# Performance work log

Hardware: AMD Instinct MI355X
Metric: run time of the kernel (lower is better)

Reference implementation:

```python
import jax, jax.numpy as jnp
import numpy as np

N_NODES = 100000
N_EDGES = 1600000
IN_DIM = 512
H0 = 32   # hiddens[0]
H1 = 8    # hiddens[1]
DH = 8    # denoise_hidden_1
ZETA = 1.01
GAMMA = 0.0


def _gcn_conv(x, row, col, edge_weight, W, b, num_nodes):
    """PyG GCNConv: add self-loops (weight 1), symmetric normalization, X@W aggregation."""
    xw = x @ W  # [N, out]
    loops = jnp.arange(num_nodes)
    r = jnp.concatenate([row, loops])
    c = jnp.concatenate([col, loops])
    w = jnp.concatenate([edge_weight, jnp.ones((num_nodes,), x.dtype)])
    deg = jax.ops.segment_sum(w, c, num_segments=num_nodes)  # degree at target nodes
    dinv = jnp.where(deg > 0, jax.lax.rsqrt(deg), 0.0)
    norm = dinv[r] * w * dinv[c]                  # [E+N]
    msg = xw[r] * norm[:, None]                   # gather source features, scale
    out = jax.ops.segment_sum(msg, c, num_segments=num_nodes)
    return out + b


def setup_inputs() -> dict:
    key = jax.random.key(0)
    ks = jax.random.split(key, 12)
    x = jax.random.normal(ks[0], (N_NODES, IN_DIM), dtype=jnp.float32)
    edge_idx = jax.random.randint(ks[1], (2, N_EDGES), 0, N_NODES, dtype=jnp.int64)

    def lin(k, fan_in, fan_out):
        bound = 1.0 / np.sqrt(fan_in)
        k1, k2 = jax.random.split(k)
        W = jax.random.uniform(k1, (fan_in, fan_out), jnp.float32, -bound, bound)
        b = jax.random.uniform(k2, (fan_out,), jnp.float32, -bound, bound)
        return W, b

    W0, b0 = lin(ks[2], IN_DIM, H0)      # outer_conv GCN weight
    W1, b1 = lin(ks[3], H0, H1)          # convs[0] GCN weight
    Wnb, bnb = lin(ks[4], H0, DH)        # nblayers[0]
    Wself, bself = lin(ks[5], H0, DH)    # selflayers[0]
    Watt, batt = lin(ks[6], 2 * DH, 1)   # attentions[0][0]
    return {"x": x, "edge_idx": edge_idx,
            "W0": W0, "b0": b0, "W1": W1, "b1": b1,
            "Wnb": Wnb, "bnb": bnb, "Wself": Wself, "bself": bself,
            "Watt": Watt, "batt": batt}


def reference(x, edge_idx, W0, b0, W1, b1, Wnb, bnb, Wself, bself, Watt, batt):
    N = x.shape[0]
    E = edge_idx.shape[1]
    row, col = edge_idx[0], edge_idx[1]

    # outer GCNConv (unit edge weights)
    h = _gcn_conv(x, row, col, jnp.ones((E,), x.dtype), W0, b0, N)  # [N, 32]

    # per-edge attention MLP: gather both endpoints, tiny 8-wide projections
    f1 = h[row] @ Wnb + bnb        # [E, 8]
    f2 = h[col] @ Wself + bself    # [E, 8]
    cat = jnp.concatenate([f1, f2], axis=1)           # [E, 16]
    weight = jax.nn.relu(cat @ Watt + batt)           # [E, 1]

    # hard-concrete gate (eval path: gate_inputs = log_alpha)
    mask = jnp.clip(jax.nn.sigmoid(weight) * (ZETA - GAMMA) + GAMMA, 0.0, 1.0)  # [E, 1]
    masked_weight = (mask * weight)[:, 0]             # [E]

    # gated GCNConv; L=1 so the mean over xs is the single output
    out = _gcn_conv(h, row, col, masked_weight, W1, b1, N)  # [N, 8]
    return out
```

## Files before the change

### kernel.cpp

```cpp
#include <hip/hip_runtime.h>
#include <cstdint>

#define N_NODES 100000
#define N_EDGES 1600000
#define ZERO_NB 391
#define YD 16
#define CAP 64

__global__ __launch_bounds__(256) void k_prep(
    const float* __restrict__ W0, const float* __restrict__ b0,
    const float* __restrict__ W1,
    const float* __restrict__ Wnb, const float* __restrict__ bnb,
    const float* __restrict__ Wself, const float* __restrict__ bself,
    const float* __restrict__ Watt, const float* __restrict__ batt,
    float* __restrict__ w0m_t, float* __restrict__ kc, int* __restrict__ cnt) {
  if (blockIdx.x >= 20) {
    int i = (blockIdx.x - 20) * 256 + threadIdx.x;
    if (i < N_NODES) cnt[i] = 0;
    return;
  }
  __shared__ float M[32][10];
  int t = threadIdx.x;
  if (t < 32) {
    for (int j = 0; j < 8; ++j) M[t][j] = W1[t * 8 + j];
    float a1 = 0.f, a2 = 0.f;
    for (int j = 0; j < 8; ++j) {
      a1 += Wnb[t * 8 + j] * Watt[j];
      a2 += Wself[t * 8 + j] * Watt[8 + j];
    }
    M[t][8] = a1; M[t][9] = a2;
  }
  __syncthreads();
  int o = blockIdx.x * 256 + t;
  int j = o >> 9, k = o & 511;
  float a = 0.f;
  for (int m = 0; m < 32; ++m) a += W0[k * 32 + m] * M[m][j];
  w0m_t[o] = a;
  if (blockIdx.x == 0) {
    if (t < 10) {
      float b = 0.f;
      for (int m = 0; m < 32; ++m) b += b0[m] * M[m][t];
      if (t == 8) { for (int jj = 0; jj < 8; ++jj) b += bnb[jj] * Watt[jj]; b += batt[0]; }
      if (t == 9) { for (int jj = 0; jj < 8; ++jj) b += bself[jj] * Watt[8 + jj]; }
      kc[t] = b;
    }
    if (t >= 10 && t < 12) kc[t] = 0.f;
  }
}

__global__ __launch_bounds__(256) void k_fused(const float* __restrict__ x,
                                               const float* __restrict__ w0m_t,
                                               const int* __restrict__ row,
                                               const int* __restrict__ col,
                                               int* __restrict__ cnt,
                                               int* __restrict__ bucket,
                                               float* __restrict__ y) {
  __shared__ float wl[10 * 512];
  int bt = blockIdx.x % 3;
  int bi = blockIdx.x / 3;
  if (bt != 0) {
    int sb = bi * 2 + (bt - 1);
    int e = sb * 256 + threadIdx.x;
    int c = col[e];
    int r = row[e];
    int p = atomicAdd(&cnt[c], 1);
    if (p < CAP) bucket[(c << 6) + p] = r;
    return;
  }
  {
    const float4* src = (const float4*)w0m_t;
    float4* dst = (float4*)wl;
    for (int f = threadIdx.x; f < 1280; f += 256) dst[f] = src[f];
  }
  __syncthreads();
  const int lane = threadIdx.x & 63;
  const int wave = (bi << 2) + (threadIdx.x >> 6);
  const int p = lane & 7;
  const int rsub = lane >> 3;
  const int rowi = wave * 8 + rsub;
  const float* xr = x + (size_t)rowi * 512;
  float acc[10];
#pragma unroll
  for (int j = 0; j < 10; ++j) acc[j] = 0.f;
#pragma unroll 4
  for (int it = 0; it < 16; ++it) {
    const int k0 = it * 32 + p * 4;
    float4 xv = *(const float4*)(xr + k0);
#pragma unroll
    for (int j = 0; j < 10; ++j) {
      float4 wv = *(const float4*)&wl[j * 512 + k0];
      acc[j] += xv.x * wv.x + xv.y * wv.y + xv.z * wv.z + xv.w * wv.w;
    }
  }
#pragma unroll
  for (int d = 1; d < 8; d <<= 1)
#pragma unroll
    for (int j = 0; j < 10; ++j) acc[j] += __shfl_xor(acc[j], d, 64);
  float* yp = y + ((size_t)rowi << 4);
  if (p == 0) {
    *(float4*)yp       = make_float4(acc[0], acc[1], acc[2], acc[3]);
    *(float4*)(yp + 4) = make_float4(acc[4], acc[5], acc[6], acc[7]);
  } else if (p == 1) {
    *(float4*)(yp + 8) = make_float4(acc[8], acc[9], 0.f, 0.f);
  }
}

__global__ __launch_bounds__(256) void k_fill_d(const int* __restrict__ cnt,
                                                float* __restrict__ y) {
  int i = blockIdx.x * 256 + threadIdx.x;
  if (i >= N_NODES) return;
  y[((size_t)i << 4) + 10] = rsqrtf((float)cnt[i] + 1.0f);
}

__global__ __launch_bounds__(256) void k_agg1(const int* __restrict__ cnt,
                                              const int* __restrict__ bucket,
                                              const float* __restrict__ y,
                                              const float* __restrict__ kc,
                                              float* __restrict__ hw,
                                              float* __restrict__ s1c,
                                              float* __restrict__ s2c) {
  int tid = blockIdx.x * 256 + threadIdx.x;
  if (tid >= N_NODES * 2) return;
  int i = tid >> 1, h = tid & 1;
  int cn = cnt[i]; if (cn > CAP) cn = CAP;
  int p0 = i << 6, p1 = p0 + cn;
  float a0 = 0.f, a1 = 0.f, a2 = 0.f, a3 = 0.f;
  float a4 = 0.f, a5 = 0.f, a6 = 0.f, a7 = 0.f;
  float a8 = 0.f, a9 = 0.f;
  for (int p = p0 + h; p < p1; p += 2) {
    int r = bucket[p];
    const float* yr = y + ((size_t)r << 4);
    float4 v0 = *(const float4*)yr;
    float4 v1 = *(const float4*)(yr + 4);
    float4 v2 = *(const float4*)(yr + 8);
    float dr = v2.z;
    a0 += v0.x * dr; a1 += v0.y * dr; a2 += v0.z * dr; a3 += v0.w * dr;
    a4 += v1.x * dr; a5 += v1.y * dr; a6 += v1.z * dr; a7 += v1.w * dr;
    a8 += v2.x * dr; a9 += v2.y * dr;
  }
  a0 += __shfl_xor(a0, 1, 64); a1 += __shfl_xor(a1, 1, 64);
  a2 += __shfl_xor(a2, 1, 64); a3 += __shfl_xor(a3, 1, 64);
  a4 += __shfl_xor(a4, 1, 64); a5 += __shfl_xor(a5, 1, 64);
  a6 += __shfl_xor(a6, 1, 64); a7 += __shfl_xor(a7, 1, 64);
  a8 += __shfl_xor(a8, 1, 64); a9 += __shfl_xor(a9, 1, 64);
  const float* yi = y + ((size_t)i << 4);
  float di = yi[10];
  if (h == 0) {
    float4 sv = *(const float4*)yi;
    float4 kq = *(const float4*)(kc);
    *(float4*)(hw + (size_t)i * 8) =
        make_float4(di * (a0 + di * sv.x) + kq.x, di * (a1 + di * sv.y) + kq.y,
                    di * (a2 + di * sv.z) + kq.z, di * (a3 + di * sv.w) + kq.w);
    s1c[i] = di * (a8 + di * yi[8]) + kc[8];
  } else {
    float4 sv = *(const float4*)(yi + 4);
    float4 kq = *(const float4*)(kc + 4);
    *(float4*)(hw + (size_t)i * 8 + 4) =
        make_float4(di * (a4 + di * sv.x) + kq.x, di * (a5 + di * sv.y) + kq.y,
                    di * (a6 + di * sv.z) + kq.z, di * (a7 + di * sv.w) + kq.w);
    s2c[i] = di * (a9 + di * yi[9]) + kc[9];
  }
}

__global__ __launch_bounds__(256) void k_gate(const int* __restrict__ cnt,
                                              const int* __restrict__ bucket,
                                              const float* __restrict__ s1c,
                                              const float* __restrict__ s2c,
                                              float* __restrict__ e2,
                                              float* __restrict__ dinv2,
                                              float* __restrict__ hw) {
  int tid = blockIdx.x * 256 + threadIdx.x;
  if (tid >= N_NODES * 2) return;
  int i = tid >> 1, h = tid & 1;
  int cn = cnt[i]; if (cn > CAP) cn = CAP;
  int p0 = i << 6, p1 = p0 + cn;
  float s2i = s2c[i];
  float sum = 0.f;
  for (int p = p0 + h; p < p1; p += 2) {
    int r = bucket[p];
    float w = fmaxf(s1c[r] + s2i, 0.f);
    float m = fminf(1.01f / (1.f + __expf(-w)), 1.f);
    float mw = m * w;
    ((float2*)e2)[p] = make_float2(__int_as_float(r), mw);
    sum += mw;
  }
  sum += __shfl_xor(sum, 1, 64);
  float di = rsqrtf(sum + 1.0f);
  if (h == 0) dinv2[i] = di;
  float4* hp = (float4*)(hw + (size_t)i * 8 + h * 4);
  float4 hv = *hp;
  *hp = make_float4(hv.x * di, hv.y * di, hv.z * di, hv.w * di);
}

__global__ __launch_bounds__(256) void k_conv2g(const int* __restrict__ cnt,
                                                const float* __restrict__ e2,
                                                const float* __restrict__ hw,
                                                const float* __restrict__ dinv2,
                                                const float* __restrict__ b1,
                                                float* __restrict__ out) {
  int tid = blockIdx.x * 256 + threadIdx.x;
  if (tid >= N_NODES * 2) return;
  int i = tid >> 1, h = tid & 1;
  int cn = cnt[i]; if (cn > CAP) cn = CAP;
  int p0 = i << 6, p1 = p0 + cn;
  float di = dinv2[i];
  float a0 = 0.f, a1 = 0.f, a2 = 0.f, a3 = 0.f;
  float a4 = 0.f, a5 = 0.f, a6 = 0.f, a7 = 0.f;
  for (int p = p0 + h; p < p1; p += 2) {
    float2 e = ((const float2*)e2)[p];
    int r = __float_as_int(e.x);
    float c = e.y;
    const float* hr = hw + ((size_t)r << 3);
    float4 v0 = *(const float4*)hr;
    float4 v1 = *(const float4*)(hr + 4);
    a0 += v0.x * c; a1 += v0.y * c; a2 += v0.z * c; a3 += v0.w * c;
    a4 += v1.x * c; a5 += v1.y * c; a6 += v1.z * c; a7 += v1.w * c;
  }
  a0 += __shfl_xor(a0, 1, 64); a1 += __shfl_xor(a1, 1, 64);
  a2 += __shfl_xor(a2, 1, 64); a3 += __shfl_xor(a3, 1, 64);
  a4 += __shfl_xor(a4, 1, 64); a5 += __shfl_xor(a5, 1, 64);
  a6 += __shfl_xor(a6, 1, 64); a7 += __shfl_xor(a7, 1, 64);
  const float* hi = hw + ((size_t)i << 3);
  if (h == 0) {
    float4 sv = *(const float4*)hi;
    float4 bq = *(const float4*)b1;
    *(float4*)(out + (size_t)i * 8) =
        make_float4(di * (a0 + sv.x) + bq.x, di * (a1 + sv.y) + bq.y,
                    di * (a2 + sv.z) + bq.z, di * (a3 + sv.w) + bq.w);
  } else {
    float4 sv = *(const float4*)(hi + 4);
    float4 bq = *(const float4*)(b1 + 4);
    *(float4*)(out + (size_t)i * 8 + 4) =
        make_float4(di * (a4 + sv.x) + bq.x, di * (a5 + sv.y) + bq.y,
                    di * (a6 + sv.z) + bq.z, di * (a7 + sv.w) + bq.w);
  }
}

extern "C" void kernel_launch(void* const* d_in, const int* in_sizes, int n_in,
                              void* d_out, int out_size, void* d_ws, size_t ws_size,
                              hipStream_t stream) {
  const float* x     = (const float*)d_in[0];
  const int*   eidx  = (const int*)d_in[1];
  const int*   row   = eidx;
  const int*   col   = eidx + N_EDGES;
  const float* W0    = (const float*)d_in[2];
  const float* b0    = (const float*)d_in[3];
  const float* W1    = (const float*)d_in[4];
  const float* b1    = (const float*)d_in[5];
  const float* Wnb   = (const float*)d_in[6];
  const float* bnb   = (const float*)d_in[7];
  const float* Wself = (const float*)d_in[8];
  const float* bself = (const float*)d_in[9];
  const float* Watt  = (const float*)d_in[10];
  const float* batt  = (const float*)d_in[11];
  float* wsf = (float*)d_ws;

  float* y      = wsf + 0;
  float* hw     = wsf + 1600000;
  int*   bucket = (int*)(wsf + 2400000);
  float* e2     = wsf + 8800000;
  int*   cnt    = (int*)(wsf + 21600000);
  float* dinv2  = wsf + 21700000;
  float* s1c    = wsf + 21800000;
  float* s2c    = wsf + 21900000;
  float* w0m_t  = wsf + 22000000;
  float* kc     = wsf + 22005120;

  float* out = (float*)d_out;

  k_prep<<<20 + ZERO_NB, 256, 0, stream>>>(W0, b0, W1, Wnb, bnb, Wself, bself,
                                           Watt, batt, w0m_t, kc, cnt);
  k_fused<<<9375, 256, 0, stream>>>(x, w0m_t, row, col, cnt, bucket, y);
  k_fill_d<<<ZERO_NB, 256, 0, stream>>>(cnt, y);
  k_agg1<<<(N_NODES * 2 + 255) / 256, 256, 0, stream>>>(cnt, bucket, y, kc, hw, s1c, s2c);
  k_gate<<<(N_NODES * 2 + 255) / 256, 256, 0, stream>>>(cnt, bucket, s1c, s2c, e2, dinv2, hw);
  k_conv2g<<<(N_NODES * 2 + 255) / 256, 256, 0, stream>>>(cnt, e2, hw, dinv2, b1, out);
}
```

Baseline: 422.9 us.

## Partition edge bucketing by destination range across interleaved blocks

The edge-bucketing blocks inside the fused kernel are reorganised so that each of 8 block slots per group handles only edges whose destination falls in one 12500-node range. Every 512-edge chunk is now scanned 8 times, and each pass does atomics only for its own range. The goal is to concentrate atomic traffic and bucket writes for concurrently running blocks into a narrower region, which may improve cache locality. In exchange, col is read 8 times, the grid grows with extra early-exit blocks, and the index arithmetic that interleaves the GEMM blocks becomes more complex.

```diff
diff --git a/kernel.cpp b/kernel.cpp
--- a/kernel.cpp
+++ b/kernel.cpp
@@ -6,6 +6,7 @@
 #define ZERO_NB 391
 #define YD 16
 #define CAP 64
+#define SC_RANGE 12500
 
 __global__ __launch_bounds__(256) void k_prep(
     const float* __restrict__ W0, const float* __restrict__ b0,
@@ -56,17 +57,32 @@
                                                int* __restrict__ bucket,
                                                float* __restrict__ y) {
   __shared__ float wl[10 * 512];
-  int bt = blockIdx.x % 3;
-  int bi = blockIdx.x / 3;
-  if (bt != 0) {
-    int sb = bi * 2 + (bt - 1);
-    int e = sb * 256 + threadIdx.x;
-    int c = col[e];
-    int r = row[e];
-    int p = atomicAdd(&cnt[c], 1);
-    if (p < CAP) bucket[(c << 6) + p] = r;
+  int B = blockIdx.x;
+  int g = B / 72;
+  int within = B - g * 72;
+  int m9 = within % 9;
+  if (m9 != 8) {
+    int r8 = within & 7;
+    int j = (within - r8) >> 3;
+    int j0 = (r8 + 1) % 9;
+    int rank = (j < j0) ? j : j - 1;
+    int chunk = g * 8 + rank;
+    if (chunk >= 3125) return;
+    int e0 = chunk * 512 + threadIdx.x * 2;
+    int lo = r8 * SC_RANGE, hi = lo + SC_RANGE;
+    int2 c2 = *(const int2*)(col + e0);
+    if (c2.x >= lo && c2.x < hi) {
+      int p = atomicAdd(&cnt[c2.x], 1);
+      if (p < CAP) bucket[(c2.x << 6) + p] = row[e0];
+    }
+    if (c2.y >= lo && c2.y < hi) {
+      int p = atomicAdd(&cnt[c2.y], 1);
+      if (p < CAP) bucket[(c2.y << 6) + p] = row[e0 + 1];
+    }
     return;
   }
+  int bi = g * 8 + within / 9;
+  if (bi >= 3125) return;
   {
     const float4* src = (const float4*)w0m_t;
     float4* dst = (float4*)wl;
@@ -270,7 +286,7 @@
 
   k_prep<<<20 + ZERO_NB, 256, 0, stream>>>(W0, b0, W1, Wnb, bnb, Wself, bself,
                                            Watt, batt, w0m_t, kc, cnt);
-  k_fused<<<9375, 256, 0, stream>>>(x, w0m_t, row, col, cnt, bucket, y);
+  k_fused<<<391 * 72, 256, 0, stream>>>(x, w0m_t, row, col, cnt, bucket, y);
   k_fill_d<<<ZERO_NB, 256, 0, stream>>>(cnt, y);
   k_agg1<<<(N_NODES * 2 + 255) / 256, 256, 0, stream>>>(cnt, bucket, y, kc, hw, s1c, s2c);
   k_gate<<<(N_NODES * 2 + 255) / 256, 256, 0, stream>>>(cnt, bucket, s1c, s2c, e2, dinv2, hw);
```

New measurement: 468.6 us. 10.8% more time.
